# Kernel optimization log

Hardware: AMD Instinct MI355X
Metric: run time of the kernel (lower is better)

Reference implementation:

```python
import jax, jax.numpy as jnp
import numpy as np

N = 50000      # nodes
E = 800000     # edges
INIT = 256     # input feature dim
HID = 64       # per-head hidden dim
EMB = 128      # output embed dim
H = 8          # heads
ALPHA = 0.2    # leaky-relu slope
EPS = 1e-16    # guard for isolated nodes


def setup_inputs() -> dict:
    key = jax.random.key(0)
    ks = jax.random.split(key, 6)
    x = jax.random.normal(ks[0], (N, INIT), dtype=jnp.float32)
    edge_index = jax.random.randint(ks[1], (2, E), 0, N, dtype=jnp.int32)
    # xavier-ish scaling keeps exp(-leakyrelu(.)) in a sane range
    W1 = jax.random.normal(ks[2], (H, INIT, HID), dtype=jnp.float32) / np.sqrt(INIT).astype(np.float32)
    a1 = jax.random.normal(ks[3], (H, 2 * HID), dtype=jnp.float32) / np.sqrt(2 * HID).astype(np.float32)
    Wo = jax.random.normal(ks[4], (H * HID, EMB), dtype=jnp.float32) / np.sqrt(H * HID).astype(np.float32)
    ao = jax.random.normal(ks[5], (2 * EMB,), dtype=jnp.float32) / np.sqrt(2 * EMB).astype(np.float32)
    return {"x": x, "edge_index": edge_index, "W1": W1, "a1": a1, "Wo": Wo, "ao": ao}


def _sp_att_head(x, W, a, src, dst):
    """One sparse GAT head (pyGAT SpGraphAttentionLayer math)."""
    h = x @ W                                              # [N, F']
    eh = jnp.concatenate([h[src], h[dst]], axis=1)          # [E, 2F']
    ee = jnp.exp(-jax.nn.leaky_relu(eh @ a, ALPHA))         # [E]
    denom = jax.ops.segment_sum(ee, src, num_segments=N) + EPS          # [N]
    num = jax.ops.segment_sum(ee[:, None] * h[dst], src, num_segments=N)  # [N, F']
    h_prime = num / denom[:, None]
    att = ee / denom[src]
    return h_prime, att


def reference(x, edge_index, W1, a1, Wo, ao, args=0):
    src, dst = edge_index[0], edge_index[1]
    # first (and only) multi-head layer, concat=True -> elu per head, concat on feature dim
    heads = [jax.nn.elu(_sp_att_head(x, W1[i], a1[i], src, dst)[0]) for i in range(H)]
    x1 = jnp.concatenate(heads, axis=1)                     # [N, H*HID]
    # output attention layer, concat=False; top-level applies elu
    h_prime, att_out = _sp_att_head(x1, Wo, ao, src, dst)
    return jax.nn.elu(h_prime), edge_index, att_out
```

## Files before the change

kernel.cpp:

```cpp
#include <hip/hip_runtime.h>
#include <hip/hip_bf16.h>
#include <cstddef>

#define NN    50000
#define NE    800000
#define FIN   256
#define HID   64
#define NH    8
#define F1    512
#define EMB   128
#define ALPHA 0.2f
#define EPSF  1e-16f
#define NBLK  ((NN + 255) / 256)

#if defined(__has_builtin)
# if __has_builtin(__builtin_amdgcn_cvt_scalef32_pk_f32_fp4) && __has_builtin(__builtin_amdgcn_cvt_scalef32_pk_fp4_f32)
#  define HAVE_FP4 1
# else
#  define HAVE_FP4 0
# endif
#else
# define HAVE_FP4 0
#endif

typedef __hip_bfloat16 bf16;
typedef __attribute__((ext_vector_type(8))) short short8;
typedef __attribute__((ext_vector_type(4))) float f32x4;
typedef __attribute__((ext_vector_type(2))) float f32x2;

#if HAVE_FP4
typedef uint2 pay_t;
#define PAYB1 (F1 / 2)
#define PAYB2 (EMB / 2)
#define SINV1 2.0f
#define SINV2 4.0f
#define PSC1  0.5f
#define PSC2  0.25f
#else
typedef uint4 pay_t;
#define PAYB1 F1
#define PAYB2 EMB
#define SINV1 1.0f
#define SINV2 1.0f
#define PSC1  1.0f
#define PSC2  1.0f
#endif

__device__ __forceinline__ float eluf(float x){ return x > 0.f ? x : expm1f(x); }
__device__ __forceinline__ float lrelu_neg_exp(float s){
    float lr = s > 0.f ? s : ALPHA * s;
    return __expf(-lr);
}
__device__ __forceinline__ float b2f(unsigned u){ return __uint_as_float(u << 16); }

__device__ __forceinline__ void fma16pk(f32x2* acc, pay_t q, float e){
    f32x2 e2; e2[0] = e; e2[1] = e;
#if HAVE_FP4
    acc[0] += __builtin_amdgcn_cvt_scalef32_pk_f32_fp4(q.x, 1.0f, 0) * e2;
    acc[1] += __builtin_amdgcn_cvt_scalef32_pk_f32_fp4(q.x, 1.0f, 1) * e2;
    acc[2] += __builtin_amdgcn_cvt_scalef32_pk_f32_fp4(q.x, 1.0f, 2) * e2;
    acc[3] += __builtin_amdgcn_cvt_scalef32_pk_f32_fp4(q.x, 1.0f, 3) * e2;
    acc[4] += __builtin_amdgcn_cvt_scalef32_pk_f32_fp4(q.y, 1.0f, 0) * e2;
    acc[5] += __builtin_amdgcn_cvt_scalef32_pk_f32_fp4(q.y, 1.0f, 1) * e2;
    acc[6] += __builtin_amdgcn_cvt_scalef32_pk_f32_fp4(q.y, 1.0f, 2) * e2;
    acc[7] += __builtin_amdgcn_cvt_scalef32_pk_f32_fp4(q.y, 1.0f, 3) * e2;
#else
    acc[0] += __builtin_amdgcn_cvt_pk_f32_fp8(q.x, false) * e2;
    acc[1] += __builtin_amdgcn_cvt_pk_f32_fp8(q.x, true)  * e2;
    acc[2] += __builtin_amdgcn_cvt_pk_f32_fp8(q.y, false) * e2;
    acc[3] += __builtin_amdgcn_cvt_pk_f32_fp8(q.y, true)  * e2;
    acc[4] += __builtin_amdgcn_cvt_pk_f32_fp8(q.z, false) * e2;
    acc[5] += __builtin_amdgcn_cvt_pk_f32_fp8(q.z, true)  * e2;
    acc[6] += __builtin_amdgcn_cvt_pk_f32_fp8(q.w, false) * e2;
    acc[7] += __builtin_amdgcn_cvt_pk_f32_fp8(q.w, true)  * e2;
#endif
}

__device__ __forceinline__ unsigned bpack(float a, float b){
    unsigned ua = __float_as_uint(a), ub = __float_as_uint(b);
    ua = (ua + 0x7fffu + ((ua >> 16) & 1)) >> 16;
    ub = (ub + 0x7fffu + ((ub >> 16) & 1)) >> 16;
    return (ua & 0xffffu) | (ub << 16);
}

__global__ void k_tw1(const float* __restrict__ W1, bf16* __restrict__ Bt1){
    int i = blockIdx.x * 256 + threadIdx.x;
    if (i >= F1 * FIN) return;
    int n = i >> 8, k = i & 255;
    Bt1[i] = __float2bfloat16(W1[(size_t)(n >> 6) * FIN * HID + (size_t)k * HID + (n & 63)]);
}

__global__ void k_tw2(const float* __restrict__ Wo, bf16* __restrict__ WoT){
    int i = blockIdx.x * 256 + threadIdx.x;
    if (i >= EMB * F1) return;
    int n = i >> 9, k = i & 511;
    WoT[i] = __float2bfloat16(Wo[(size_t)k * EMB + n]);
}

__global__ void k_q4(const unsigned char* __restrict__ in, unsigned* __restrict__ out,
                     int n8, float sinv){
    int i = blockIdx.x * 256 + threadIdx.x;
    if (i >= n8) return;
    uint2 v = *(const uint2*)(in + (size_t)i * 8);
#if HAVE_FP4
    f32x2 a = __builtin_amdgcn_cvt_pk_f32_fp8(v.x, false);
    f32x2 b = __builtin_amdgcn_cvt_pk_f32_fp8(v.x, true);
    f32x2 c = __builtin_amdgcn_cvt_pk_f32_fp8(v.y, false);
    f32x2 d = __builtin_amdgcn_cvt_pk_f32_fp8(v.y, true);
    unsigned r = 0;
    r = __builtin_amdgcn_cvt_scalef32_pk_fp4_f32(r, a[0] * sinv, a[1] * sinv, 1.0f, 0);
    r = __builtin_amdgcn_cvt_scalef32_pk_fp4_f32(r, b[0] * sinv, b[1] * sinv, 1.0f, 1);
    r = __builtin_amdgcn_cvt_scalef32_pk_fp4_f32(r, c[0] * sinv, c[1] * sinv, 1.0f, 2);
    r = __builtin_amdgcn_cvt_scalef32_pk_fp4_f32(r, d[0] * sinv, d[1] * sinv, 1.0f, 3);
    out[i] = r;
#else
    (void)sinv;
    *(uint2*)((unsigned char*)out + (size_t)i * 8) = v;
#endif
}

__global__ void k_zero(int* p, int n){
    int i = blockIdx.x * 256 + threadIdx.x;
    if (i < n) p[i] = 0;
}

__global__ void k_count(const int* __restrict__ src, int* __restrict__ cnt){
    int e = blockIdx.x * 256 + threadIdx.x;
    if (e < NE) atomicAdd(&cnt[src[e]], 1);
}

__global__ __launch_bounds__(256) void k_bsum(const int* __restrict__ cnt, int* __restrict__ bsum){
    const int b = blockIdx.x, t = threadIdx.x, idx = b * 256 + t;
    int v = (idx < NN) ? cnt[idx] : 0;
#pragma unroll
    for (int o = 1; o < 64; o <<= 1) v += __shfl_xor(v, o);
    __shared__ int ws[4];
    if ((t & 63) == 0) ws[t >> 6] = v;
    __syncthreads();
    if (t == 0) bsum[b] = ws[0] + ws[1] + ws[2] + ws[3];
}

__global__ __launch_bounds__(256) void k_scanb(const int* __restrict__ bsum,
                                               int* __restrict__ boff,
                                               int* __restrict__ rp){
    const int t = threadIdx.x;
    __shared__ int s[256];
    const int v = (t < NBLK) ? bsum[t] : 0;
    s[t] = v;
    __syncthreads();
    for (int o = 1; o < 256; o <<= 1){
        int u = (t >= o) ? s[t - o] : 0;
        __syncthreads();
        s[t] += u;
        __syncthreads();
    }
    if (t < NBLK) boff[t] = s[t] - v;
    if (t == 255) rp[NN] = s[255];
}

__global__ __launch_bounds__(256) void k_rp(const int* __restrict__ cnt,
                                            const int* __restrict__ boff,
                                            int* __restrict__ rp){
    const int b = blockIdx.x, t = threadIdx.x, idx = b * 256 + t;
    const int v = (idx < NN) ? cnt[idx] : 0;
    __shared__ int s[256];
    s[t] = v;
    __syncthreads();
    for (int o = 1; o < 256; o <<= 1){
        int u = (t >= o) ? s[t - o] : 0;
        __syncthreads();
        s[t] += u;
        __syncthreads();
    }
    if (idx < NN) rp[idx] = boff[b] + s[t] - v;
}

__global__ void k_scatter(const int* __restrict__ src, const int* __restrict__ dst,
                          const int* __restrict__ rp, int* __restrict__ cur,
                          int* __restrict__ sdst){
    int e = blockIdx.x * 256 + threadIdx.x;
    if (e < NE){
        int s = src[e];
        int p = atomicAdd(&cur[s], 1);
        sdst[rp[s] + p] = dst[e];
    }
}

__global__ __launch_bounds__(256) void k_gemm1f(const float* __restrict__ A,
                                                const bf16* __restrict__ B,
                                                unsigned char* __restrict__ C){
    constexpr int K = FIN, N = F1;
    constexpr int LDT = 40;
    __shared__ __align__(16) bf16 As[128 * LDT];
    __shared__ __align__(16) bf16 Bs[128 * LDT];
    const int t = threadIdx.x;
    const int lane = t & 63, wid = t >> 6;
    const int m0 = blockIdx.x * 128, n0 = blockIdx.y * 128;
    const int r0 = t >> 2, u0 = t & 3;
    const int r1 = r0 + 64;
    const int rb = (wid & 1) * 64, cb = (wid >> 1) * 64;
    const int fr = lane & 15, fk = (lane >> 4) * 8;

    f32x4 acc[4][4];
#pragma unroll
    for (int i = 0; i < 4; i++)
#pragma unroll
        for (int j = 0; j < 4; j++) acc[i][j] = (f32x4)(0.f);

    for (int k0 = 0; k0 < K; k0 += 32){
        const int ga0 = m0 + r0, ga1 = m0 + r1;
        float4 a0a = make_float4(0,0,0,0), a0b = a0a, a1a = a0a, a1b = a0a;
        if (ga0 < NN){
            const float* p = A + (size_t)ga0 * K + k0 + u0 * 8;
            a0a = *(const float4*)p; a0b = *(const float4*)(p + 4);
        }
        if (ga1 < NN){
            const float* p = A + (size_t)ga1 * K + k0 + u0 * 8;
            a1a = *(const float4*)p; a1b = *(const float4*)(p + 4);
        }
        uint4 av0, av1;
        av0.x = bpack(a0a.x, a0a.y); av0.y = bpack(a0a.z, a0a.w);
        av0.z = bpack(a0b.x, a0b.y); av0.w = bpack(a0b.z, a0b.w);
        av1.x = bpack(a1a.x, a1a.y); av1.y = bpack(a1a.z, a1a.w);
        av1.z = bpack(a1b.x, a1b.y); av1.w = bpack(a1b.z, a1b.w);
        uint4 bv0 = *(const uint4*)(B + (size_t)(n0 + r0) * K + k0 + u0 * 8);
        uint4 bv1 = *(const uint4*)(B + (size_t)(n0 + r1) * K + k0 + u0 * 8);
        __syncthreads();
        *(uint4*)(As + r0 * LDT + u0 * 8) = av0;
        *(uint4*)(As + r1 * LDT + u0 * 8) = av1;
        *(uint4*)(Bs + r0 * LDT + u0 * 8) = bv0;
        *(uint4*)(Bs + r1 * LDT + u0 * 8) = bv1;
        __syncthreads();
        short8 af[4], bf_[4];
#pragma unroll
        for (int i = 0; i < 4; i++){
            af[i]  = *(const short8*)(As + (rb + i * 16 + fr) * LDT + fk);
            bf_[i] = *(const short8*)(Bs + (cb + i * 16 + fr) * LDT + fk);
        }
#pragma unroll
        for (int i = 0; i < 4; i++)
#pragma unroll
            for (int j = 0; j < 4; j++)
                acc[i][j] = __builtin_amdgcn_mfma_f32_16x16x32_bf16(af[i], bf_[j], acc[i][j], 0, 0, 0);
    }
    const int crow = m0 + rb + (lane >> 4) * 4;
    const int ccol = n0 + cb + (lane & 15);
#pragma unroll
    for (int i = 0; i < 4; i++)
#pragma unroll
        for (int j = 0; j < 4; j++)
#pragma unroll
            for (int v = 0; v < 4; v++){
                int row = crow + i * 16 + v;
                if (row < NN){
                    float val = acc[i][j][v];
                    unsigned r = __builtin_amdgcn_cvt_pk_fp8_f32(val, val, 0u, false);
                    C[(size_t)row * N + ccol + j * 16] = (unsigned char)(r & 0xffu);
                }
            }
}

template<int K>
__global__ __launch_bounds__(256) void k_mgemm(const bf16* __restrict__ A,
                                               const bf16* __restrict__ B,
                                               unsigned char* __restrict__ C,
                                               int N){
    constexpr int LDT = 40;
    __shared__ __align__(16) bf16 As[128 * LDT];
    __shared__ __align__(16) bf16 Bs[128 * LDT];
    const int t = threadIdx.x;
    const int lane = t & 63, wid = t >> 6;
    const int m0 = blockIdx.x * 128, n0 = blockIdx.y * 128;
    const int r0 = t >> 2, u0 = t & 3;
    const int r1 = r0 + 64;
    const int rb = (wid & 1) * 64, cb = (wid >> 1) * 64;
    const int fr = lane & 15, fk = (lane >> 4) * 8;

    f32x4 acc[4][4];
#pragma unroll
    for (int i = 0; i < 4; i++)
#pragma unroll
        for (int j = 0; j < 4; j++) acc[i][j] = (f32x4)(0.f);

    for (int k0 = 0; k0 < K; k0 += 32){
        const int ga0 = m0 + r0, ga1 = m0 + r1;
        uint4 av0 = (ga0 < NN) ? *(const uint4*)(A + (size_t)ga0 * K + k0 + u0 * 8)
                               : make_uint4(0, 0, 0, 0);
        uint4 av1 = (ga1 < NN) ? *(const uint4*)(A + (size_t)ga1 * K + k0 + u0 * 8)
                               : make_uint4(0, 0, 0, 0);
        uint4 bv0 = *(const uint4*)(B + (size_t)(n0 + r0) * K + k0 + u0 * 8);
        uint4 bv1 = *(const uint4*)(B + (size_t)(n0 + r1) * K + k0 + u0 * 8);
        __syncthreads();
        *(uint4*)(As + r0 * LDT + u0 * 8) = av0;
        *(uint4*)(As + r1 * LDT + u0 * 8) = av1;
        *(uint4*)(Bs + r0 * LDT + u0 * 8) = bv0;
        *(uint4*)(Bs + r1 * LDT + u0 * 8) = bv1;
        __syncthreads();
        short8 af[4], bf_[4];
#pragma unroll
        for (int i = 0; i < 4; i++){
            af[i]  = *(const short8*)(As + (rb + i * 16 + fr) * LDT + fk);
            bf_[i] = *(const short8*)(Bs + (cb + i * 16 + fr) * LDT + fk);
        }
#pragma unroll
        for (int i = 0; i < 4; i++)
#pragma unroll
            for (int j = 0; j < 4; j++)
                acc[i][j] = __builtin_amdgcn_mfma_f32_16x16x32_bf16(af[i], bf_[j], acc[i][j], 0, 0, 0);
    }
    const int crow = m0 + rb + (lane >> 4) * 4;
    const int ccol = n0 + cb + (lane & 15);
#pragma unroll
    for (int i = 0; i < 4; i++)
#pragma unroll
        for (int j = 0; j < 4; j++)
#pragma unroll
            for (int v = 0; v < 4; v++){
                int row = crow + i * 16 + v;
                if (row < NN){
                    float val = acc[i][j][v];
                    unsigned r = __builtin_amdgcn_cvt_pk_fp8_f32(val, val, 0u, false);
                    C[(size_t)row * N + ccol + j * 16] = (unsigned char)(r & 0xffu);
                }
            }
}

__global__ void k_s1q(const unsigned char* __restrict__ h1q, const float* __restrict__ a1,
                      float* __restrict__ s11, float* __restrict__ s12,
                      unsigned char* __restrict__ pay){
    int idx = blockIdx.x * 256 + threadIdx.x;
    if (idx >= NN * NH) return;
    int n = idx >> 3, h = idx & 7;
    const uint4* hp = (const uint4*)(h1q + (size_t)n * F1 + h * HID);
    const float* a  = a1 + (size_t)h * 2 * HID;
    float d1 = 0.f, d2 = 0.f;
    float f[64];
#pragma unroll
    for (int u = 0; u < 4; u++){
        uint4 q = hp[u];
        int j = u * 16;
        f32x2 p;
        p = __builtin_amdgcn_cvt_pk_f32_fp8(q.x, false); f[j+0]=p[0];  f[j+1]=p[1];
        p = __builtin_amdgcn_cvt_pk_f32_fp8(q.x, true);  f[j+2]=p[0];  f[j+3]=p[1];
        p = __builtin_amdgcn_cvt_pk_f32_fp8(q.y, false); f[j+4]=p[0];  f[j+5]=p[1];
        p = __builtin_amdgcn_cvt_pk_f32_fp8(q.y, true);  f[j+6]=p[0];  f[j+7]=p[1];
        p = __builtin_amdgcn_cvt_pk_f32_fp8(q.z, false); f[j+8]=p[0];  f[j+9]=p[1];
        p = __builtin_amdgcn_cvt_pk_f32_fp8(q.z, true);  f[j+10]=p[0]; f[j+11]=p[1];
        p = __builtin_amdgcn_cvt_pk_f32_fp8(q.w, false); f[j+12]=p[0]; f[j+13]=p[1];
        p = __builtin_amdgcn_cvt_pk_f32_fp8(q.w, true);  f[j+14]=p[0]; f[j+15]=p[1];
    }
#pragma unroll
    for (int j = 0; j < 64; j++){
        d1 += f[j] * a[j];
        d2 += f[j] * a[HID + j];
    }
    s11[idx] = d1;
    s12[idx] = d2;
#if HAVE_FP4
    unsigned r[4];
#pragma unroll
    for (int u = 0; u < 4; u++){
        unsigned rr = 0;
        int j = u * 16;
        rr = __builtin_amdgcn_cvt_scalef32_pk_fp4_f32(rr, f[j+0]*SINV1,  f[j+1]*SINV1,  1.0f, 0);
        rr = __builtin_amdgcn_cvt_scalef32_pk_fp4_f32(rr, f[j+2]*SINV1,  f[j+3]*SINV1,  1.0f, 1);
        rr = __builtin_amdgcn_cvt_scalef32_pk_fp4_f32(rr, f[j+4]*SINV1,  f[j+5]*SINV1,  1.0f, 2);
        rr = __builtin_amdgcn_cvt_scalef32_pk_fp4_f32(rr, f[j+6]*SINV1,  f[j+7]*SINV1,  1.0f, 3);
        r[u] = rr;
        (void)j;
    }
    unsigned w8[8];
#pragma unroll
    for (int u = 0; u < 8; u++){
        unsigned rr = 0;
        int j = u * 8;
        rr = __builtin_amdgcn_cvt_scalef32_pk_fp4_f32(rr, f[j+0]*SINV1, f[j+1]*SINV1, 1.0f, 0);
        rr = __builtin_amdgcn_cvt_scalef32_pk_fp4_f32(rr, f[j+2]*SINV1, f[j+3]*SINV1, 1.0f, 1);
        rr = __builtin_amdgcn_cvt_scalef32_pk_fp4_f32(rr, f[j+4]*SINV1, f[j+5]*SINV1, 1.0f, 2);
        rr = __builtin_amdgcn_cvt_scalef32_pk_fp4_f32(rr, f[j+6]*SINV1, f[j+7]*SINV1, 1.0f, 3);
        w8[u] = rr;
    }
    uint4* op = (uint4*)(pay + (size_t)n * PAYB1 + h * (HID / 2));
    uint4 o0, o1;
    o0.x = w8[0]; o0.y = w8[1]; o0.z = w8[2]; o0.w = w8[3];
    o1.x = w8[4]; o1.y = w8[5]; o1.z = w8[6]; o1.w = w8[7];
    op[0] = o0; op[1] = o1;
#else
    uint4* op = (uint4*)(pay + (size_t)n * PAYB1 + h * HID);
    op[0] = hp[0]; op[1] = hp[1]; op[2] = hp[2]; op[3] = hp[3];
#endif
}

__global__ __launch_bounds__(256) void k_agg1(const unsigned char* __restrict__ hq,
                                              const float* __restrict__ s11,
                                              const float* __restrict__ s12,
                                              const int* __restrict__ rp,
                                              const int* __restrict__ sdst,
                                              bf16* __restrict__ x1){
    const int t = threadIdx.x, lane = t & 63, w = t >> 6;
    const int n = blockIdx.x * 4 + w;
    const int ha = lane & 7;
    const int l32 = lane & 31;
    const int half = lane >> 5;
    const int hf = l32 >> 2;
    const int es = lane >> 3;
    const float s1a = s11[n * NH + ha];
    f32x2 acc[8];
#pragma unroll
    for (int i = 0; i < 8; i++){ acc[i][0] = 0.f; acc[i][1] = 0.f; }
    float dedp = 0.f;
    const int start = rp[n], end = rp[n + 1];
    const unsigned char* __restrict__ hl = hq + (size_t)l32 * (PAYB1 / 32);
    for (int c0 = start; c0 < end; c0 += 64){
        const int m = min(64, end - c0);
        int dreg = (lane < m) ? sdst[c0 + lane] : 0;
        for (int sc = 0; sc < m; sc += 8){
            const int el = sc + es;
            const int de = __shfl(dreg, el);
            const float ev = (el < m) ? lrelu_neg_exp(s1a + s12[de * NH + ha]) : 0.f;
            dedp += ev;
#pragma unroll
            for (int p = 0; p < 4; p++){
                const float ej = __shfl(ev, ((2 * p + half) << 3) + hf);
                const int   dj = __shfl(dreg, sc + 2 * p + half);
                pay_t q = *(const pay_t*)(hl + (size_t)dj * PAYB1);
                fma16pk(acc, q, ej);
            }
        }
    }
    dedp += __shfl_xor(dedp, 8);
    dedp += __shfl_xor(dedp, 16);
    dedp += __shfl_xor(dedp, 32);
#pragma unroll
    for (int i = 0; i < 8; i++){
        acc[i][0] += __shfl_xor(acc[i][0], 32);
        acc[i][1] += __shfl_xor(acc[i][1], 32);
    }
    float ded = __shfl(dedp, hf);
    const float inv = PSC1 / (ded + EPSF);
    if (half == 0){
        float o[16];
#pragma unroll
        for (int i = 0; i < 8; i++){
            o[2 * i]     = eluf(acc[i][0] * inv);
            o[2 * i + 1] = eluf(acc[i][1] * inv);
        }
        uint4 ov0, ov1;
        ov0.x = bpack(o[0], o[1]);   ov0.y = bpack(o[2], o[3]);
        ov0.z = bpack(o[4], o[5]);   ov0.w = bpack(o[6], o[7]);
        ov1.x = bpack(o[8], o[9]);   ov1.y = bpack(o[10], o[11]);
        ov1.z = bpack(o[12], o[13]); ov1.w = bpack(o[14], o[15]);
        bf16* xp = x1 + (size_t)n * F1 + l32 * 16;
        *(uint4*)xp = ov0;
        *(uint4*)(xp + 8) = ov1;
    }
}

__global__ void k_s2(const unsigned char* __restrict__ h2q, const float* __restrict__ ao,
                     float* __restrict__ s21, float* __restrict__ s22){
    int n = blockIdx.x * 256 + threadIdx.x;
    if (n >= NN) return;
    const uint4* hp = (const uint4*)(h2q + (size_t)n * EMB);
    float d1 = 0.f, d2 = 0.f;
#pragma unroll
    for (int u = 0; u < 8; u++){
        uint4 q = hp[u];
        int j = u * 16;
#define S2(w, o) { f32x2 p0 = __builtin_amdgcn_cvt_pk_f32_fp8((w), false); \
                   f32x2 p1 = __builtin_amdgcn_cvt_pk_f32_fp8((w), true); \
                   d1 += p0[0]*ao[(o)] + p0[1]*ao[(o)+1] + p1[0]*ao[(o)+2] + p1[1]*ao[(o)+3]; \
                   d2 += p0[0]*ao[EMB+(o)] + p0[1]*ao[EMB+(o)+1] + p1[0]*ao[EMB+(o)+2] + p1[1]*ao[EMB+(o)+3]; }
        S2(q.x, j) S2(q.y, j + 4) S2(q.z, j + 8) S2(q.w, j + 12)
#undef S2
    }
    s21[n] = d1;
    s22[n] = d2;
}

__global__ __launch_bounds__(256) void k_agg2(const unsigned char* __restrict__ hq,
                                              const float* __restrict__ s21,
                                              const float* __restrict__ s22,
                                              const int* __restrict__ rp,
                                              const int* __restrict__ sdst,
                                              float* __restrict__ den2,
                                              float* __restrict__ out0){
    const int t = threadIdx.x, lane = t & 63, w = t >> 6;
    const int n = blockIdx.x * 4 + w;
    const int slot = lane >> 3;
    const int fpos = lane & 7;
    const float s1v = s21[n];
    f32x2 acc[8];
#pragma unroll
    for (int i = 0; i < 8; i++){ acc[i][0] = 0.f; acc[i][1] = 0.f; }
    float dedp = 0.f;
    const int start = rp[n], end = rp[n + 1];
    const unsigned char* __restrict__ hl = hq + (size_t)fpos * (PAYB2 / 8);
    for (int c0 = start; c0 < end; c0 += 64){
        const int m = min(64, end - c0);
        int dreg = (lane < m) ? sdst[c0 + lane] : 0;
        float ev = (lane < m) ? lrelu_neg_exp(s1v + s22[dreg]) : 0.f;
        dedp += ev;
        for (int j = 0; j < m; j += 8){
            const int ei = j + slot;
            const float e = __shfl(ev, ei);
            const int   d = __shfl(dreg, ei);
            pay_t q = *(const pay_t*)(hl + (size_t)d * PAYB2);
            fma16pk(acc, q, e);
        }
    }
#pragma unroll
    for (int o = 1; o <= 32; o <<= 1) dedp += __shfl_xor(dedp, o);
#pragma unroll
    for (int o = 8; o <= 32; o <<= 1)
#pragma unroll
        for (int i = 0; i < 8; i++){
            acc[i][0] += __shfl_xor(acc[i][0], o);
            acc[i][1] += __shfl_xor(acc[i][1], o);
        }
    const float den = dedp + EPSF;
    if (slot == 0){
        const float inv = PSC2 / den;
        float* op = out0 + (size_t)n * EMB + fpos * 16;
#pragma unroll
        for (int u = 0; u < 4; u++){
            float4 ov;
            ov.x = eluf(acc[2 * u][0] * inv);
            ov.y = eluf(acc[2 * u][1] * inv);
            ov.z = eluf(acc[2 * u + 1][0] * inv);
            ov.w = eluf(acc[2 * u + 1][1] * inv);
            *(float4*)(op + u * 4) = ov;
        }
        if (lane == 0) den2[n] = den;
    }
}

__global__ void k_att_edge(const int* __restrict__ ei,
                           const float* __restrict__ s21, const float* __restrict__ s22,
                           const float* __restrict__ den2,
                           float* __restrict__ outE, float* __restrict__ outA){
    int i = blockIdx.x * 256 + threadIdx.x;
    if (i < 2 * NE) outE[i] = (float)ei[i];
    if (i < NE){
        int s = ei[i], d = ei[NE + i];
        float ee = lrelu_neg_exp(s21[s] + s22[d]);
        outA[i] = ee / den2[s];
    }
}

extern "C" void kernel_launch(void* const* d_in, const int* in_sizes, int n_in,
                              void* d_out, int out_size, void* d_ws, size_t ws_size,
                              hipStream_t stream){
    const float* x  = (const float*)d_in[0];
    const int*   ei = (const int*)d_in[1];
    const float* W1 = (const float*)d_in[2];
    const float* a1 = (const float*)d_in[3];
    const float* Wo = (const float*)d_in[4];
    const float* ao = (const float*)d_in[5];
    float* out = (float*)d_out;
    const int* src = ei;
    const int* dst = ei + NE;

    char* w = (char*)d_ws;
    auto alloc = [&](size_t bytes) -> char* {
        char* p = w;
        w += (bytes + 255) & ~(size_t)255;
        return p;
    };
    unsigned char* h1pay = (unsigned char*)alloc((size_t)NN * F1);
    bf16*  x1   = (bf16*) alloc((size_t)NN * F1 * 2);
    unsigned char* h1q = (unsigned char*)alloc((size_t)NN * F1);
    unsigned char* h2q = (unsigned char*)alloc((size_t)NN * EMB);
    bf16*  Bt1  = (bf16*) alloc((size_t)F1 * FIN * 2);
    bf16*  WoT  = (bf16*) alloc((size_t)EMB * F1 * 2);
    float* s11  = (float*)alloc((size_t)NN * NH * 4);
    float* s12  = (float*)alloc((size_t)NN * NH * 4);
    float* s21  = (float*)alloc((size_t)NN * 4);
    float* s22  = (float*)alloc((size_t)NN * 4);
    float* den2 = (float*)alloc((size_t)NN * 4);
    int*   cnt2 = (int*)  alloc((size_t)2 * NN * 4);
    int*   rp   = (int*)  alloc((size_t)(NN + 1) * 4);
    int*   sdst = (int*)  alloc((size_t)NE * 4);
    int*   bsum = (int*)  alloc((size_t)NBLK * 4);
    int*   boff = (int*)  alloc((size_t)NBLK * 4);
    int*   cnt = cnt2;
    int*   cur = cnt2 + NN;
    unsigned char* h2pay = (unsigned char*)x1;

    k_tw1<<<(F1 * FIN + 255) / 256, 256, 0, stream>>>(W1, Bt1);
    k_tw2<<<(EMB * F1 + 255) / 256, 256, 0, stream>>>(Wo, WoT);

    k_zero   <<<(2 * NN + 255) / 256, 256, 0, stream>>>(cnt2, 2 * NN);
    k_count  <<<(NE + 255) / 256,     256, 0, stream>>>(src, cnt);
    k_bsum   <<<NBLK,                 256, 0, stream>>>(cnt, bsum);
    k_scanb  <<<1,                    256, 0, stream>>>(bsum, boff, rp);
    k_rp     <<<NBLK,                 256, 0, stream>>>(cnt, boff, rp);
    k_scatter<<<(NE + 255) / 256,     256, 0, stream>>>(src, dst, rp, cur, sdst);

    k_gemm1f<<<dim3((NN + 127) / 128, F1 / 128), 256, 0, stream>>>(x, Bt1, h1q);
    k_s1q <<<(NN * NH + 255) / 256, 256, 0, stream>>>(h1q, a1, s11, s12, h1pay);
    k_agg1<<<NN / 4, 256, 0, stream>>>(h1pay, s11, s12, rp, sdst, x1);

    k_mgemm<F1><<<dim3((NN + 127) / 128, EMB / 128), 256, 0, stream>>>(x1, WoT, h2q, EMB);
    k_q4  <<<(NN * EMB / 8 + 255) / 256, 256, 0, stream>>>(h2q, (unsigned*)h2pay, NN * EMB / 8, SINV2);
    k_s2  <<<(NN + 255) / 256, 256, 0, stream>>>(h2q, ao, s21, s22);
    k_agg2<<<NN / 4, 256, 0, stream>>>(h2pay, s21, s22, rp, sdst, den2, out);

    k_att_edge<<<(2 * NE + 255) / 256, 256, 0, stream>>>(ei, s21, s22, den2,
                                                         out + (size_t)NN * EMB,
                                                         out + (size_t)NN * EMB + 2 * NE);
}
```

Measured before the change: 321.3 us.

## Precompute per-edge layer-1 attention weights and batch gathers in aggregation

Adds a k_ee pass that computes the eight per-head edge weights once per edge from s11/s12 and stores them as packed bf16. The scatter kernel now also writes a CSR-ordered source array for that pass. k_agg1 reads these weights instead of doing the s12 gather and exp inline, and issues eight payload loads before consuming them to raise memory-level parallelism. It also swaps expm1f for __expf-1 in ELU and drops an unused fp4 pack loop. The cost is an extra kernel launch plus roughly 13 MB of edge-weight traffic, bf16 rounding of the weights, and reduced accuracy of ELU near zero.

```diff
diff --git a/kernel.cpp b/kernel.cpp
--- a/kernel.cpp
+++ b/kernel.cpp
@@ -46,7 +46,7 @@
 #define PSC2  1.0f
 #endif
 
-__device__ __forceinline__ float eluf(float x){ return x > 0.f ? x : expm1f(x); }
+__device__ __forceinline__ float eluf(float x){ return x > 0.f ? x : __expf(x) - 1.f; }
 __device__ __forceinline__ float lrelu_neg_exp(float s){
     float lr = s > 0.f ? s : ALPHA * s;
     return __expf(-lr);
@@ -177,13 +177,31 @@
 
 __global__ void k_scatter(const int* __restrict__ src, const int* __restrict__ dst,
                           const int* __restrict__ rp, int* __restrict__ cur,
-                          int* __restrict__ sdst){
+                          int* __restrict__ sdst, int* __restrict__ ssrc){
     int e = blockIdx.x * 256 + threadIdx.x;
     if (e < NE){
         int s = src[e];
         int p = atomicAdd(&cur[s], 1);
         sdst[rp[s] + p] = dst[e];
-    }
+        ssrc[rp[s] + p] = s;
+    }
+}
+
+__global__ void k_ee(const int* __restrict__ ssrc, const int* __restrict__ sdst,
+                     const float* __restrict__ s11, const float* __restrict__ s12,
+                     unsigned short* __restrict__ ee8b){
+    int i = blockIdx.x * 256 + threadIdx.x;
+    if (i >= NE) return;
+    int s = ssrc[i], d = sdst[i];
+    const float* ps = s11 + (size_t)s * NH;
+    const float* pd = s12 + (size_t)d * NH;
+    float e[8];
+#pragma unroll
+    for (int h = 0; h < 8; h++) e[h] = lrelu_neg_exp(ps[h] + pd[h]);
+    uint4 o;
+    o.x = bpack(e[0], e[1]); o.y = bpack(e[2], e[3]);
+    o.z = bpack(e[4], e[5]); o.w = bpack(e[6], e[7]);
+    *(uint4*)(ee8b + (size_t)i * 8) = o;
 }
 
 __global__ __launch_bounds__(256) void k_gemm1f(const float* __restrict__ A,
@@ -357,18 +375,6 @@
     s11[idx] = d1;
     s12[idx] = d2;
 #if HAVE_FP4
-    unsigned r[4];
-#pragma unroll
-    for (int u = 0; u < 4; u++){
-        unsigned rr = 0;
-        int j = u * 16;
-        rr = __builtin_amdgcn_cvt_scalef32_pk_fp4_f32(rr, f[j+0]*SINV1,  f[j+1]*SINV1,  1.0f, 0);
-        rr = __builtin_amdgcn_cvt_scalef32_pk_fp4_f32(rr, f[j+2]*SINV1,  f[j+3]*SINV1,  1.0f, 1);
-        rr = __builtin_amdgcn_cvt_scalef32_pk_fp4_f32(rr, f[j+4]*SINV1,  f[j+5]*SINV1,  1.0f, 2);
-        rr = __builtin_amdgcn_cvt_scalef32_pk_fp4_f32(rr, f[j+6]*SINV1,  f[j+7]*SINV1,  1.0f, 3);
-        r[u] = rr;
-        (void)j;
-    }
     unsigned w8[8];
 #pragma unroll
     for (int u = 0; u < 8; u++){
@@ -392,19 +398,16 @@
 }
 
 __global__ __launch_bounds__(256) void k_agg1(const unsigned char* __restrict__ hq,
-                                              const float* __restrict__ s11,
-                                              const float* __restrict__ s12,
+                                              const unsigned short* __restrict__ ee8b,
                                               const int* __restrict__ rp,
                                               const int* __restrict__ sdst,
                                               bf16* __restrict__ x1){
     const int t = threadIdx.x, lane = t & 63, w = t >> 6;
     const int n = blockIdx.x * 4 + w;
-    const int ha = lane & 7;
     const int l32 = lane & 31;
     const int half = lane >> 5;
     const int hf = l32 >> 2;
-    const int es = lane >> 3;
-    const float s1a = s11[n * NH + ha];
+    const int eslot = lane >> 3;
     f32x2 acc[8];
 #pragma unroll
     for (int i = 0; i < 8; i++){ acc[i][0] = 0.f; acc[i][1] = 0.f; }
@@ -414,17 +417,24 @@
     for (int c0 = start; c0 < end; c0 += 64){
         const int m = min(64, end - c0);
         int dreg = (lane < m) ? sdst[c0 + lane] : 0;
-        for (int sc = 0; sc < m; sc += 8){
-            const int el = sc + es;
-            const int de = __shfl(dreg, el);
-            const float ev = (el < m) ? lrelu_neg_exp(s1a + s12[de * NH + ha]) : 0.f;
-            dedp += ev;
-#pragma unroll
-            for (int p = 0; p < 4; p++){
-                const float ej = __shfl(ev, ((2 * p + half) << 3) + hf);
-                const int   dj = __shfl(dreg, sc + 2 * p + half);
-                pay_t q = *(const pay_t*)(hl + (size_t)dj * PAYB1);
-                fma16pk(acc, q, ej);
+        for (int g = 0; g * 8 < m; g++){
+            unsigned short eu = ee8b[(size_t)(c0 + g * 8) * 8 + lane];
+            dedp += (g * 8 + eslot < m) ? b2f(eu) : 0.f;
+        }
+        for (int j = 0; j < m; j += 16){
+            int dj[8]; unsigned short eu[8]; pay_t q[8];
+#pragma unroll
+            for (int p = 0; p < 8; p++){
+                const int e2 = j + 2 * p + half;
+                dj[p] = __shfl(dreg, e2);
+                eu[p] = ee8b[(size_t)(c0 + e2) * 8 + hf];
+                q[p]  = *(const pay_t*)(hl + (size_t)dj[p] * PAYB1);
+            }
+#pragma unroll
+            for (int p = 0; p < 8; p++){
+                const int e2 = j + 2 * p + half;
+                const float e = (e2 < m) ? b2f(eu[p]) : 0.f;
+                fma16pk(acc, q[p], e);
             }
         }
     }
@@ -570,6 +580,7 @@
     bf16*  x1   = (bf16*) alloc((size_t)NN * F1 * 2);
     unsigned char* h1q = (unsigned char*)alloc((size_t)NN * F1);
     unsigned char* h2q = (unsigned char*)alloc((size_t)NN * EMB);
+    unsigned short* ee8b = (unsigned short*)alloc(((size_t)NE + 64) * 8 * 2);
     bf16*  Bt1  = (bf16*) alloc((size_t)F1 * FIN * 2);
     bf16*  WoT  = (bf16*) alloc((size_t)EMB * F1 * 2);
     float* s11  = (float*)alloc((size_t)NN * NH * 4);
@@ -580,6 +591,7 @@
     int*   cnt2 = (int*)  alloc((size_t)2 * NN * 4);
     int*   rp   = (int*)  alloc((size_t)(NN + 1) * 4);
     int*   sdst = (int*)  alloc((size_t)NE * 4);
+    int*   ssrc = (int*)  alloc((size_t)NE * 4);
     int*   bsum = (int*)  alloc((size_t)NBLK * 4);
     int*   boff = (int*)  alloc((size_t)NBLK * 4);
     int*   cnt = cnt2;
@@ -594,11 +606,12 @@
     k_bsum   <<<NBLK,                 256, 0, stream>>>(cnt, bsum);
     k_scanb  <<<1,                    256, 0, stream>>>(bsum, boff, rp);
     k_rp     <<<NBLK,                 256, 0, stream>>>(cnt, boff, rp);
-    k_scatter<<<(NE + 255) / 256,     256, 0, stream>>>(src, dst, rp, cur, sdst);
+    k_scatter<<<(NE + 255) / 256,     256, 0, stream>>>(src, dst, rp, cur, sdst, ssrc);
 
     k_gemm1f<<<dim3((NN + 127) / 128, F1 / 128), 256, 0, stream>>>(x, Bt1, h1q);
     k_s1q <<<(NN * NH + 255) / 256, 256, 0, stream>>>(h1q, a1, s11, s12, h1pay);
-    k_agg1<<<NN / 4, 256, 0, stream>>>(h1pay, s11, s12, rp, sdst, x1);
+    k_ee  <<<(NE + 255) / 256, 256, 0, stream>>>(ssrc, sdst, s11, s12, ee8b);
+    k_agg1<<<NN / 4, 256, 0, stream>>>(h1pay, ee8b, rp, sdst, x1);
 
     k_mgemm<F1><<<dim3((NN + 127) / 128, EMB / 128), 256, 0, stream>>>(x1, WoT, h2q, EMB);
     k_q4  <<<(NN * EMB / 8 + 255) / 256, 256, 0, stream>>>(h2q, (unsigned*)h2pay, NN * EMB / 8, SINV2);
```

After: 335.8 us. 1.05x slower.
